# Optimization experiments

Hardware: AMD Instinct MI355X
Metric: run time of the kernel (lower is better)

Reference implementation:

```python
import jax, jax.numpy as jnp
import numpy as np

VOCAB = 32000
HIDDEN = 1024
BATCH = 4
SEQ = 2048


def setup_inputs() -> dict:
    key = jax.random.key(0)
    k_ids, k_w, k_b = jax.random.split(key, 3)
    input_ids = jax.random.randint(k_ids, (BATCH, SEQ), 0, VOCAB, dtype=jnp.int64 if jax.config.jax_enable_x64 else jnp.int32)
    # torch nn.Linear(vocab, hidden): weight [hidden, vocab], bias [hidden]
    W = jax.random.normal(k_w, (HIDDEN, VOCAB), dtype=jnp.float32) * (1.0 / np.sqrt(VOCAB))
    b = jax.random.normal(k_b, (HIDDEN,), dtype=jnp.float32) * 0.02
    return {"input_ids": input_ids, "W": W, "b": b}


def reference(input_ids, W, b):
    # Faithful to the original: one-hot the ids then run the dense Linear.
    # E: [B, S, V] one-hot float, out = E @ W^T + b -> [B, S, H]
    E = jax.nn.one_hot(input_ids, VOCAB, dtype=jnp.float32)
    X = jnp.einsum("bsv,hv->bsh", E, W) + b
    return X
```

## Files before the change

kernel.cpp:

```cpp
#include <hip/hip_runtime.h>


#define VOCAB   32000
#define HIDDEN  1024
#define CBIN    256
#define NBIN    125
#define ROWS    64
#define NCH     (HIDDEN/ROWS)
#define WCAP    256
#define NTOK    8192

__device__ __forceinline__ float bf2f(unsigned short h) {
    return __uint_as_float((unsigned)h << 16);
}
__device__ __forceinline__ unsigned pack2(float a, float b) {
    unsigned ua = __float_as_uint(a) + 0x8000u;
    unsigned ub = __float_as_uint(b) + 0x8000u;
    return __builtin_amdgcn_perm(ub, ua, 0x07060302u);
}

__global__ __launch_bounds__(256, 4) void fused_onehot_kernel(
    const int* __restrict__ ids,
    const float* __restrict__ W,
    const float* __restrict__ b,
    float* __restrict__ out)
{
    const int bin = blockIdx.x;
    const int c0  = bin * CBIN;
    const int h0  = blockIdx.y * ROWS;
    const int t   = threadIdx.x;
    const int w   = t >> 6;
    const int lane = t & 63;

    __shared__ unsigned short tile[ROWS * CBIN];
    __shared__ int m_s[4 * WCAP];
    __shared__ int wcnt_s[4];
    __shared__ int ovf_s[4];

    const int c4 = (t & 63) * 4;
    const int r0 = t >> 6;
    float4 wv[16];
    #pragma unroll
    for (int i = 0; i < 16; ++i) {
        const int r = r0 + 4 * i;
        wv[i] = *reinterpret_cast<const float4*>(
            &W[(size_t)(h0 + r) * VOCAB + c0 + c4]);
    }

    if (lane == 0) { wcnt_s[w] = 0; ovf_s[w] = 0; }
    const unsigned long long lt = (1ull << lane) - 1ull;
    int wcnt = 0;
    #pragma unroll
    for (int sp = 0; sp < 4; ++sp) {
        const int4* p = reinterpret_cast<const int4*>(ids + sp * 2048) + t * 2;
        const int4 a = p[0], e = p[1];
        const int v[8] = {a.x, a.y, a.z, a.w, e.x, e.y, e.z, e.w};
        #pragma unroll
        for (int k = 0; k < 8; ++k) {
            const int d = v[k] - c0;
            const bool hit = (unsigned)d < (unsigned)CBIN;
            const unsigned long long mm = __ballot(hit);
            if (hit) {
                const int idx = wcnt + __popcll(mm & lt);
                if (idx < WCAP)
                    m_s[w * WCAP + idx] = ((sp * 2048 + t * 8 + k) << 8) | d;
                else
                    ovf_s[w] = 1;
                (void)0;
            }
            wcnt += (int)__popcll(mm);
        }
    }
    if (lane == 0) wcnt_s[w] = wcnt;

    #pragma unroll
    for (int i = 0; i < 16; ++i) {
        const int r  = r0 + 4 * i;
        const int cs = (c4 + (r & ~3)) & 255;
        *reinterpret_cast<uint2*>(&tile[r * CBIN + cs]) =
            make_uint2(pack2(wv[i].x, wv[i].y), pack2(wv[i].z, wv[i].w));
    }

    __syncthreads();

    const int g  = t & 15;
    const int q  = t >> 4;
    const int r4 = g * 4;
    const float4 bv = *reinterpret_cast<const float4*>(&b[h0 + r4]);

    #pragma unroll
    for (int ws = 0; ws < 4; ++ws) {
        const int cnt = min(wcnt_s[ws], WCAP);
        for (int j = q; j < cnt; j += 16) {
            const int m   = m_s[ws * WCAP + j];
            const int tok = m >> 8;
            const int d   = m & 255;
            const int cs  = (d + r4) & 255;
            float4 o;
            o.x = bf2f(tile[(r4 + 0) * CBIN + cs]) + bv.x;
            o.y = bf2f(tile[(r4 + 1) * CBIN + cs]) + bv.y;
            o.z = bf2f(tile[(r4 + 2) * CBIN + cs]) + bv.z;
            o.w = bf2f(tile[(r4 + 3) * CBIN + cs]) + bv.w;
            *reinterpret_cast<float4*>(&out[(size_t)tok * HIDDEN + h0 + r4]) = o;
        }
    }

    if (ovf_s[w]) {
        int rc = 0;
        for (int sp = 0; sp < 4; ++sp) {
            const int4* p = reinterpret_cast<const int4*>(ids + sp * 2048) + t * 2;
            const int4 a = p[0], e = p[1];
            const int v[8] = {a.x, a.y, a.z, a.w, e.x, e.y, e.z, e.w};
            for (int k = 0; k < 8; ++k) {
                const int d = v[k] - c0;
                const bool hit = (unsigned)d < (unsigned)CBIN;
                const unsigned long long mm = __ballot(hit);
                if (hit) {
                    const int idx = rc + __popcll(mm & lt);
                    if (idx >= WCAP) {
                        const int tok = sp * 2048 + t * 8 + k;
                        for (int r = 0; r < ROWS; ++r) {
                            const int cs2 = (d + (r & ~3)) & 255;
                            out[(size_t)tok * HIDDEN + h0 + r] =
                                bf2f(tile[r * CBIN + cs2]) + b[h0 + r];
                        }
                    }
                }
                rc += (int)__popcll(mm);
            }
        }
    }
}

__global__ __launch_bounds__(256) void fallback_kernel(
    const int* __restrict__ ids, const float* __restrict__ W,
    const float* __restrict__ b, float* __restrict__ out, int n_tokens)
{
    const int t = threadIdx.x;
    const int sub = t >> 6, lane = t & 63;
    const int token = blockIdx.x * 4 + sub;
    if (token >= n_tokens) return;
    const int id = ids[token];
    const float* Wcol = W + (size_t)id;
    float v[16];
    #pragma unroll
    for (int j = 0; j < 4; ++j) {
        const int h0 = j * 256 + lane * 4;
        #pragma unroll
        for (int k = 0; k < 4; ++k)
            v[j * 4 + k] = Wcol[(size_t)(h0 + k) * VOCAB];
    }
    float* orow = out + (size_t)token * HIDDEN;
    #pragma unroll
    for (int j = 0; j < 4; ++j) {
        const int h0 = j * 256 + lane * 4;
        const float4 bv = *reinterpret_cast<const float4*>(&b[h0]);
        float4 o;
        o.x = v[j*4+0] + bv.x; o.y = v[j*4+1] + bv.y;
        o.z = v[j*4+2] + bv.z; o.w = v[j*4+3] + bv.w;
        *reinterpret_cast<float4*>(&orow[h0]) = o;
    }
}

extern "C" void kernel_launch(void* const* d_in, const int* in_sizes, int n_in,
                              void* d_out, int out_size, void* d_ws, size_t ws_size,
                              hipStream_t stream)
{
    const int*   ids = (const int*)d_in[0];
    const float* W   = (const float*)d_in[1];
    const float* b   = (const float*)d_in[2];
    float*       out = (float*)d_out;

    const int n_tokens = in_sizes[0];

    if (n_tokens == NTOK) {
        fused_onehot_kernel<<<dim3(NBIN, NCH), dim3(256), 0, stream>>>(
            ids, W, b, out);
    } else {
        fallback_kernel<<<dim3((n_tokens + 3) / 4), dim3(256), 0, stream>>>(
            ids, W, b, out, n_tokens);
    }
}
```

Measured before the change: 33.92 us.

## Process two hidden-row chunks per block, prefetching second W chunk during first scatter

Each block now handles 128 hidden rows instead of 64, so the grid drops from 16 to 8 chunks along hidden. The token-bin scan (ballot/compaction of ids) is done once and reused for both chunks. The second chunk's W loads are issued before the first chunk's output scatter so their latency overlaps the stores. This halves the block count and the repeated id scans, but adds register pressure from holding 16 extra float4 values and two more barriers, and it lowers parallelism.

```diff
diff --git a/kernel.cpp b/kernel.cpp
--- a/kernel.cpp
+++ b/kernel.cpp
@@ -6,7 +6,7 @@
 #define CBIN    256
 #define NBIN    125
 #define ROWS    64
-#define NCH     (HIDDEN/ROWS)
+#define NPAIR   8
 #define WCAP    256
 #define NTOK    8192
 
@@ -25,11 +25,11 @@
     const float* __restrict__ b,
     float* __restrict__ out)
 {
-    const int bin = blockIdx.x;
-    const int c0  = bin * CBIN;
-    const int h0  = blockIdx.y * ROWS;
-    const int t   = threadIdx.x;
-    const int w   = t >> 6;
+    const int bin  = blockIdx.x;
+    const int c0   = bin * CBIN;
+    const int h0   = blockIdx.y * (2 * ROWS);
+    const int t    = threadIdx.x;
+    const int w    = t >> 6;
     const int lane = t & 63;
 
     __shared__ unsigned short tile[ROWS * CBIN];
@@ -39,6 +39,7 @@
 
     const int c4 = (t & 63) * 4;
     const int r0 = t >> 6;
+
     float4 wv[16];
     #pragma unroll
     for (int i = 0; i < 16; ++i) {
@@ -66,7 +67,6 @@
                     m_s[w * WCAP + idx] = ((sp * 2048 + t * 8 + k) << 8) | d;
                 else
                     ovf_s[w] = 1;
-                (void)0;
             }
             wcnt += (int)__popcll(mm);
         }
@@ -83,25 +83,37 @@
 
     __syncthreads();
 
+    float4 wb[16];
+    #pragma unroll
+    for (int i = 0; i < 16; ++i) {
+        const int r = r0 + 4 * i;
+        wb[i] = *reinterpret_cast<const float4*>(
+            &W[(size_t)(h0 + ROWS + r) * VOCAB + c0 + c4]);
+    }
+    __builtin_amdgcn_sched_barrier(0);
+
     const int g  = t & 15;
     const int q  = t >> 4;
     const int r4 = g * 4;
-    const float4 bv = *reinterpret_cast<const float4*>(&b[h0 + r4]);
-
-    #pragma unroll
-    for (int ws = 0; ws < 4; ++ws) {
-        const int cnt = min(wcnt_s[ws], WCAP);
-        for (int j = q; j < cnt; j += 16) {
-            const int m   = m_s[ws * WCAP + j];
-            const int tok = m >> 8;
-            const int d   = m & 255;
-            const int cs  = (d + r4) & 255;
-            float4 o;
-            o.x = bf2f(tile[(r4 + 0) * CBIN + cs]) + bv.x;
-            o.y = bf2f(tile[(r4 + 1) * CBIN + cs]) + bv.y;
-            o.z = bf2f(tile[(r4 + 2) * CBIN + cs]) + bv.z;
-            o.w = bf2f(tile[(r4 + 3) * CBIN + cs]) + bv.w;
-            *reinterpret_cast<float4*>(&out[(size_t)tok * HIDDEN + h0 + r4]) = o;
+
+    {
+        const float4 bv = *reinterpret_cast<const float4*>(&b[h0 + r4]);
+        #pragma unroll
+        for (int ws = 0; ws < 4; ++ws) {
+            const int cnt = min(wcnt_s[ws], WCAP);
+            for (int j = q; j < cnt; j += 16) {
+                const int m   = m_s[ws * WCAP + j];
+                const int tok = m >> 8;
+                const int d   = m & 255;
+                const int cs  = (d + r4) & 255;
+                float4 o;
+                o.x = bf2f(tile[(r4 + 0) * CBIN + cs]) + bv.x;
+                o.y = bf2f(tile[(r4 + 1) * CBIN + cs]) + bv.y;
+                o.z = bf2f(tile[(r4 + 2) * CBIN + cs]) + bv.z;
+                o.w = bf2f(tile[(r4 + 3) * CBIN + cs]) + bv.w;
+                *reinterpret_cast<float4*>(
+                    &out[(size_t)tok * HIDDEN + h0 + r4]) = o;
+            }
         }
     }
 
@@ -130,6 +142,64 @@
             }
         }
     }
+
+    __syncthreads();
+
+    #pragma unroll
+    for (int i = 0; i < 16; ++i) {
+        const int r  = r0 + 4 * i;
+        const int cs = (c4 + (r & ~3)) & 255;
+        *reinterpret_cast<uint2*>(&tile[r * CBIN + cs]) =
+            make_uint2(pack2(wb[i].x, wb[i].y), pack2(wb[i].z, wb[i].w));
+    }
+    __syncthreads();
+
+    {
+        const float4 bv = *reinterpret_cast<const float4*>(&b[h0 + ROWS + r4]);
+        #pragma unroll
+        for (int ws = 0; ws < 4; ++ws) {
+            const int cnt = min(wcnt_s[ws], WCAP);
+            for (int j = q; j < cnt; j += 16) {
+                const int m   = m_s[ws * WCAP + j];
+                const int tok = m >> 8;
+                const int d   = m & 255;
+                const int cs  = (d + r4) & 255;
+                float4 o;
+                o.x = bf2f(tile[(r4 + 0) * CBIN + cs]) + bv.x;
+                o.y = bf2f(tile[(r4 + 1) * CBIN + cs]) + bv.y;
+                o.z = bf2f(tile[(r4 + 2) * CBIN + cs]) + bv.z;
+                o.w = bf2f(tile[(r4 + 3) * CBIN + cs]) + bv.w;
+                *reinterpret_cast<float4*>(
+                    &out[(size_t)tok * HIDDEN + h0 + ROWS + r4]) = o;
+            }
+        }
+    }
+
+    if (ovf_s[w]) {
+        int rc = 0;
+        for (int sp = 0; sp < 4; ++sp) {
+            const int4* p = reinterpret_cast<const int4*>(ids + sp * 2048) + t * 2;
+            const int4 a = p[0], e = p[1];
+            const int v[8] = {a.x, a.y, a.z, a.w, e.x, e.y, e.z, e.w};
+            for (int k = 0; k < 8; ++k) {
+                const int d = v[k] - c0;
+                const bool hit = (unsigned)d < (unsigned)CBIN;
+                const unsigned long long mm = __ballot(hit);
+                if (hit) {
+                    const int idx = rc + __popcll(mm & lt);
+                    if (idx >= WCAP) {
+                        const int tok = sp * 2048 + t * 8 + k;
+                        for (int r = 0; r < ROWS; ++r) {
+                            const int cs2 = (d + (r & ~3)) & 255;
+                            out[(size_t)tok * HIDDEN + h0 + ROWS + r] =
+                                bf2f(tile[r * CBIN + cs2]) + b[h0 + ROWS + r];
+                        }
+                    }
+                }
+                rc += (int)__popcll(mm);
+            }
+        }
+    }
 }
 
 __global__ __launch_bounds__(256) void fallback_kernel(
@@ -174,7 +244,7 @@
     const int n_tokens = in_sizes[0];
 
     if (n_tokens == NTOK) {
-        fused_onehot_kernel<<<dim3(NBIN, NCH), dim3(256), 0, stream>>>(
+        fused_onehot_kernel<<<dim3(NBIN, NPAIR), dim3(256), 0, stream>>>(
             ids, W, b, out);
     } else {
         fallback_kernel<<<dim3((n_tokens + 3) / 4), dim3(256), 0, stream>>>(
```

Result: faster. 31.78 us (-6.3%).

## Process four hidden-row tiles per block and prefetch the next W tile

Applied to the files above, without the earlier changes.

Each block now covers 256 hidden rows in four 64-row tiles instead of one, so the grid shrinks from 125x16 to 125x4. The id scan and bin compaction are amortized across four tiles. The next tile's W rows are loaded into registers while the current tile is scattered to the output. The cost is fewer blocks (500) and therefore less parallelism, plus extra barriers between tiles.

```diff
diff --git a/kernel.cpp b/kernel.cpp
--- a/kernel.cpp
+++ b/kernel.cpp
@@ -6,7 +6,8 @@
 #define CBIN    256
 #define NBIN    125
 #define ROWS    64
-#define NCH     (HIDDEN/ROWS)
+#define NTILE   4
+#define NPART   4
 #define WCAP    256
 #define NTOK    8192
 
@@ -25,11 +26,11 @@
     const float* __restrict__ b,
     float* __restrict__ out)
 {
-    const int bin = blockIdx.x;
-    const int c0  = bin * CBIN;
-    const int h0  = blockIdx.y * ROWS;
-    const int t   = threadIdx.x;
-    const int w   = t >> 6;
+    const int bin  = blockIdx.x;
+    const int c0   = bin * CBIN;
+    const int h0   = blockIdx.y * (NTILE * ROWS);
+    const int t    = threadIdx.x;
+    const int w    = t >> 6;
     const int lane = t & 63;
 
     __shared__ unsigned short tile[ROWS * CBIN];
@@ -39,7 +40,9 @@
 
     const int c4 = (t & 63) * 4;
     const int r0 = t >> 6;
+
     float4 wv[16];
+
     #pragma unroll
     for (int i = 0; i < 16; ++i) {
         const int r = r0 + 4 * i;
@@ -66,69 +69,89 @@
                     m_s[w * WCAP + idx] = ((sp * 2048 + t * 8 + k) << 8) | d;
                 else
                     ovf_s[w] = 1;
-                (void)0;
             }
             wcnt += (int)__popcll(mm);
         }
     }
     if (lane == 0) wcnt_s[w] = wcnt;
-
-    #pragma unroll
-    for (int i = 0; i < 16; ++i) {
-        const int r  = r0 + 4 * i;
-        const int cs = (c4 + (r & ~3)) & 255;
-        *reinterpret_cast<uint2*>(&tile[r * CBIN + cs]) =
-            make_uint2(pack2(wv[i].x, wv[i].y), pack2(wv[i].z, wv[i].w));
-    }
-
-    __syncthreads();
 
     const int g  = t & 15;
     const int q  = t >> 4;
     const int r4 = g * 4;
-    const float4 bv = *reinterpret_cast<const float4*>(&b[h0 + r4]);
-
-    #pragma unroll
-    for (int ws = 0; ws < 4; ++ws) {
-        const int cnt = min(wcnt_s[ws], WCAP);
-        for (int j = q; j < cnt; j += 16) {
-            const int m   = m_s[ws * WCAP + j];
-            const int tok = m >> 8;
-            const int d   = m & 255;
-            const int cs  = (d + r4) & 255;
-            float4 o;
-            o.x = bf2f(tile[(r4 + 0) * CBIN + cs]) + bv.x;
-            o.y = bf2f(tile[(r4 + 1) * CBIN + cs]) + bv.y;
-            o.z = bf2f(tile[(r4 + 2) * CBIN + cs]) + bv.z;
-            o.w = bf2f(tile[(r4 + 3) * CBIN + cs]) + bv.w;
-            *reinterpret_cast<float4*>(&out[(size_t)tok * HIDDEN + h0 + r4]) = o;
-        }
-    }
-
-    if (ovf_s[w]) {
-        int rc = 0;
-        for (int sp = 0; sp < 4; ++sp) {
-            const int4* p = reinterpret_cast<const int4*>(ids + sp * 2048) + t * 2;
-            const int4 a = p[0], e = p[1];
-            const int v[8] = {a.x, a.y, a.z, a.w, e.x, e.y, e.z, e.w};
-            for (int k = 0; k < 8; ++k) {
-                const int d = v[k] - c0;
-                const bool hit = (unsigned)d < (unsigned)CBIN;
-                const unsigned long long mm = __ballot(hit);
-                if (hit) {
-                    const int idx = rc + __popcll(mm & lt);
-                    if (idx >= WCAP) {
-                        const int tok = sp * 2048 + t * 8 + k;
-                        for (int r = 0; r < ROWS; ++r) {
-                            const int cs2 = (d + (r & ~3)) & 255;
-                            out[(size_t)tok * HIDDEN + h0 + r] =
-                                bf2f(tile[r * CBIN + cs2]) + b[h0 + r];
+
+    #pragma unroll
+    for (int tt = 0; tt < NTILE; ++tt) {
+        const int hb = h0 + tt * ROWS;
+
+        #pragma unroll
+        for (int i = 0; i < 16; ++i) {
+            const int r  = r0 + 4 * i;
+            const int cs = (c4 + (r & ~3)) & 255;
+            *reinterpret_cast<uint2*>(&tile[r * CBIN + cs]) =
+                make_uint2(pack2(wv[i].x, wv[i].y), pack2(wv[i].z, wv[i].w));
+        }
+        __syncthreads();
+
+        if (tt + 1 < NTILE) {
+            #pragma unroll
+            for (int i = 0; i < 16; ++i) {
+                const int r = r0 + 4 * i;
+                wv[i] = *reinterpret_cast<const float4*>(
+                    &W[(size_t)(hb + ROWS + r) * VOCAB + c0 + c4]);
+            }
+            __builtin_amdgcn_sched_barrier(0);
+        }
+
+        {
+            const float4 bv = *reinterpret_cast<const float4*>(&b[hb + r4]);
+            #pragma unroll
+            for (int ws = 0; ws < 4; ++ws) {
+                const int cnt = min(wcnt_s[ws], WCAP);
+                for (int j = q; j < cnt; j += 16) {
+                    const int m   = m_s[ws * WCAP + j];
+                    const int tok = m >> 8;
+                    const int d   = m & 255;
+                    const int cs  = (d + r4) & 255;
+                    float4 o;
+                    o.x = bf2f(tile[(r4 + 0) * CBIN + cs]) + bv.x;
+                    o.y = bf2f(tile[(r4 + 1) * CBIN + cs]) + bv.y;
+                    o.z = bf2f(tile[(r4 + 2) * CBIN + cs]) + bv.z;
+                    o.w = bf2f(tile[(r4 + 3) * CBIN + cs]) + bv.w;
+                    *reinterpret_cast<float4*>(
+                        &out[(size_t)tok * HIDDEN + hb + r4]) = o;
+                }
+            }
+        }
+
+        if (ovf_s[w]) {
+            int rc = 0;
+            for (int sp = 0; sp < 4; ++sp) {
+                const int4* p =
+                    reinterpret_cast<const int4*>(ids + sp * 2048) + t * 2;
+                const int4 a = p[0], e = p[1];
+                const int v[8] = {a.x, a.y, a.z, a.w, e.x, e.y, e.z, e.w};
+                for (int k = 0; k < 8; ++k) {
+                    const int d = v[k] - c0;
+                    const bool hit = (unsigned)d < (unsigned)CBIN;
+                    const unsigned long long mm = __ballot(hit);
+                    if (hit) {
+                        const int idx = rc + __popcll(mm & lt);
+                        if (idx >= WCAP) {
+                            const int tok = sp * 2048 + t * 8 + k;
+                            for (int r = 0; r < ROWS; ++r) {
+                                const int cs2 = (d + (r & ~3)) & 255;
+                                out[(size_t)tok * HIDDEN + hb + r] =
+                                    bf2f(tile[r * CBIN + cs2]) + b[hb + r];
+                            }
                         }
                     }
+                    rc += (int)__popcll(mm);
                 }
-                rc += (int)__popcll(mm);
-            }
-        }
+            }
+        }
+
+        if (tt + 1 < NTILE)
+            __syncthreads();
     }
 }
 
@@ -174,7 +197,7 @@
     const int n_tokens = in_sizes[0];
 
     if (n_tokens == NTOK) {
-        fused_onehot_kernel<<<dim3(NBIN, NCH), dim3(256), 0, stream>>>(
+        fused_onehot_kernel<<<dim3(NBIN, NPART), dim3(256), 0, stream>>>(
             ids, W, b, out);
     } else {
         fallback_kernel<<<dim3((n_tokens + 3) / 4), dim3(256), 0, stream>>>(
```

Result: no change. 33.75 us (-0.5%).
